# Kernel tuning notes

Measured on AMD Instinct MI355X. Metric: run time of the kernel, lower is better.

## Reference

```python
import jax, jax.numpy as jnp
import numpy as np

L, C, H = 4, 512, 8
HD = C // H

def silu(x):
    return x * jax.nn.sigmoid(x)

def layernorm(x, g, b, eps=1e-5):
    m = x.mean(-1, keepdims=True)
    v = ((x - m) ** 2).mean(-1, keepdims=True)
    return (x - m) * jax.lax.rsqrt(v + eps) * g + b

def adaln(x, t, w, b):
    # x: (N,B,C), t: (B,C), w: (2C,C), b: (2C,)
    mod = silu(t) @ w.T + b
    scale, shift = jnp.split(mod, 2, axis=-1)
    return x * (1.0 + scale[None]) + shift[None]

def embed_rotary(x, pos):
    # x: (B,N,C), pos: (B,N,C,2) with [...,0]=cos, [...,1]=sin
    cos, sin = pos[..., 0], pos[..., 1]
    x2 = jnp.stack([-x[..., 1::2], x[..., 0::2]], axis=-1).reshape(x.shape)
    return x * cos + x2 * sin

def setup_inputs() -> dict:
    key = jax.random.key(0)
    ks = jax.random.split(key, 24)
    Nq, Nkv, B = 1024, 2048, 4
    query = jax.random.normal(ks[0], (Nq, B, C), jnp.float32)
    value = jax.random.normal(ks[1], (Nkv, B, C), jnp.float32)
    diff_ts = jax.random.normal(ks[2], (B, C), jnp.float32)
    # valid rotary codes: cos/sin of random angles
    aq = jax.random.uniform(ks[3], (B, Nq, C), jnp.float32, 0.0, 2 * np.pi)
    ak = jax.random.uniform(ks[4], (B, Nkv, C), jnp.float32, 0.0, 2 * np.pi)
    query_pos = jnp.stack([jnp.cos(aq), jnp.sin(aq)], axis=-1)
    value_pos = jnp.stack([jnp.cos(ak), jnp.sin(ak)], axis=-1)
    s = 0.02
    inp = dict(query=query, value=value, diff_ts=diff_ts,
               query_pos=query_pos, value_pos=value_pos,
               aw_attn=jax.random.normal(ks[5], (L, 2 * C, C)) * s,
               ab_attn=jax.random.normal(ks[6], (L, 2 * C)) * s,
               in_w=jax.random.normal(ks[7], (L, 3 * C, C)) * s,
               in_b=jnp.zeros((L, 3 * C)),
               out_w=jax.random.normal(ks[8], (L, C, C)) * s,
               out_b=jnp.zeros((L, C)),
               ln1_g=jnp.ones((L, C)), ln1_b=jnp.zeros((L, C)),
               aw_ffn=jax.random.normal(ks[9], (L, 2 * C, C)) * s,
               ab_ffn=jax.random.normal(ks[10], (L, 2 * C)) * s,
               w1=jax.random.normal(ks[11], (L, C, C)) * s,
               b1=jnp.zeros((L, C)),
               w2=jax.random.normal(ks[12], (L, C, C)) * s,
               b2=jnp.zeros((L, C)),
               ln2_g=jnp.ones((L, C)), ln2_b=jnp.zeros((L, C)))
    return inp

def _forward(query, value, diff_ts, query_pos, value_pos,
             aw_attn, ab_attn, in_w, in_b, out_w, out_b, ln1_g, ln1_b,
             aw_ffn, ab_ffn, w1, b1, w2, b2, ln2_g, ln2_b):
    Nq, B, _ = query.shape
    Nkv = value.shape[0]
    scaling = HD ** -0.5
    outputs = []
    q = query
    for i in range(L):
        # --- cross-attention layer ---
        aq = adaln(q, diff_ts, aw_attn[i], ab_attn[i])
        wq, wk, wv = jnp.split(in_w[i], 3, axis=0)
        bq, bk, bv = jnp.split(in_b[i], 3, axis=0)
        qp = (aq @ wq.T + bq) * scaling          # (Nq,B,C)
        kp = value @ wk.T + bk                    # (Nkv,B,C)
        vp = value @ wv.T + bv
        qb = embed_rotary(qp.transpose(1, 0, 2), query_pos)  # (B,Nq,C)
        kb = embed_rotary(kp.transpose(1, 0, 2), value_pos)  # (B,Nkv,C)
        vb = vp.transpose(1, 0, 2)
        qh = qb.reshape(B, Nq, H, HD).transpose(0, 2, 1, 3)   # (B,H,Nq,HD)
        kh = kb.reshape(B, Nkv, H, HD).transpose(0, 2, 1, 3)
        vh = vb.reshape(B, Nkv, H, HD).transpose(0, 2, 1, 3)
        scores = jnp.einsum('bhqd,bhkd->bhqk', qh, kh)
        attn = jax.nn.softmax(scores, axis=-1)
        o = jnp.einsum('bhqk,bhkd->bhqd', attn, vh)
        o = o.transpose(0, 2, 1, 3).reshape(B, Nq, C).transpose(1, 0, 2)  # (Nq,B,C)
        o = o @ out_w[i].T + out_b[i]
        q = layernorm(q + o, ln1_g[i], ln1_b[i])
        # --- feedforward layer (residual uses AdaLN-modulated x) ---
        xa = adaln(q, diff_ts, aw_ffn[i], ab_ffn[i])
        h = jax.nn.relu(xa @ w1[i].T + b1[i])
        h = h @ w2[i].T + b2[i]
        q = layernorm(xa + h, ln2_g[i], ln2_b[i])
        outputs.append(q)
    return jnp.stack(outputs)  # (L, Nq, B, C)

def reference(query, value, diff_ts, query_pos, value_pos,
              aw_attn, ab_attn, in_w, in_b, out_w, out_b, ln1_g, ln1_b,
              aw_ffn, ab_ffn, w1, b1, w2, b2, ln2_g, ln2_b):
    return _forward(query, value, diff_ts, query_pos, value_pos,
                    aw_attn, ab_attn, in_w, in_b, out_w, out_b, ln1_g, ln1_b,
                    aw_ffn, ab_ffn, w1, b1, w2, b2, ln2_g, ln2_b)
```

## Files before the change

kernel.cpp:

```cpp
#include <hip/hip_runtime.h>
#include <hip/hip_bf16.h>

typedef __hip_bfloat16 bf16;
typedef __attribute__((ext_vector_type(8))) short short8;
typedef __attribute__((ext_vector_type(4))) float f32x4;

#define CDIM 512
#define BDIM 4
#define HDIM 8
#define HDQ  64
#define NQ   1024
#define NKV  2048
#define LAYERS 4
#define SPLIT 2

#if defined(__has_builtin)
#if __has_builtin(__builtin_amdgcn_global_load_lds)
#define USE_GLL 1
#endif
#endif

static __device__ __forceinline__ short f2s(float f) {
    bf16 h = __float2bfloat16(f);
    return *reinterpret_cast<short*>(&h);
}


__global__ __launch_bounds__(256) void conv_f2b(const float* __restrict__ in,
                                                bf16* __restrict__ out, int n) {
    int i = blockIdx.x * 256 + threadIdx.x;
    if (i < n) out[i] = __float2bfloat16(in[i]);
}

__global__ __launch_bounds__(256) void silu_k(const float* __restrict__ t,
                                              float* __restrict__ st) {
    int i = blockIdx.x * 256 + threadIdx.x;
    float x = t[i];
    st[i] = x / (1.f + __expf(-x));
}

__global__ __launch_bounds__(256) void modall_k(const float* __restrict__ st,
    const float* __restrict__ aw_attn, const float* __restrict__ ab_attn,
    const float* __restrict__ aw_ffn,  const float* __restrict__ ab_ffn,
    float* __restrict__ mod) {
    int idx = blockIdx.x * 256 + threadIdx.x;
    int col  = idx & 1023;
    int b    = (idx >> 10) & 3;
    int kind = (idx >> 12) & 1;
    int l    = idx >> 13;
    const float* w = (kind ? aw_ffn : aw_attn) + ((size_t)l * 1024 + col) * CDIM;
    float acc = (kind ? ab_ffn : ab_attn)[l * 1024 + col];
    const float* tb = st + b * CDIM;
    for (int k = 0; k < CDIM; ++k) acc += tb[k] * w[k];
    mod[idx] = acc;
}

__global__ __launch_bounds__(256) void adaln_k(const float* __restrict__ x,
                                               const float* __restrict__ mod,
                                               bf16* __restrict__ outb) {
    int i = blockIdx.x * 256 + threadIdx.x;
    int c = i & 511;
    int b = (i >> 9) & 3;
    outb[i] = __float2bfloat16(x[i] * (1.f + mod[b * 1024 + c]) + mod[b * 1024 + 512 + c]);
}

__global__ __launch_bounds__(256) void ln_ad_k(const float* __restrict__ x,
                                               const float* __restrict__ res,
                                               const float* __restrict__ g,
                                               const float* __restrict__ bb,
                                               const float* __restrict__ mod,
                                               float* __restrict__ ln_f,
                                               float* __restrict__ ln_f2,
                                               float* __restrict__ ad_f,
                                               bf16* __restrict__ ad_b) {
    int row = blockIdx.x;
    int t = threadIdx.x;
    size_t base = (size_t)row * CDIM;
    float v0 = x[base + t] + res[base + t];
    float v1 = x[base + t + 256] + res[base + t + 256];
    float s1 = v0 + v1;
    float s2 = v0 * v0 + v1 * v1;
    #pragma unroll
    for (int off = 32; off; off >>= 1) {
        s1 += __shfl_xor(s1, off);
        s2 += __shfl_xor(s2, off);
    }
    __shared__ float a1[4], a2[4];
    int w = t >> 6;
    if ((t & 63) == 0) { a1[w] = s1; a2[w] = s2; }
    __syncthreads();
    s1 = a1[0] + a1[1] + a1[2] + a1[3];
    s2 = a2[0] + a2[1] + a2[2] + a2[3];
    float mean = s1 * (1.f / 512.f);
    float var = s2 * (1.f / 512.f) - mean * mean;
    float rs = rsqrtf(var + 1e-5f);
    float y0 = (v0 - mean) * rs * g[t] + bb[t];
    float y1 = (v1 - mean) * rs * g[t + 256] + bb[t + 256];
    if (ln_f)  { ln_f[base + t] = y0;  ln_f[base + t + 256] = y1; }
    if (ln_f2) { ln_f2[base + t] = y0; ln_f2[base + t + 256] = y1; }
    if (mod) {
        int b = row & 3;
        float o0 = y0 * (1.f + mod[b * 1024 + t]) + mod[b * 1024 + 512 + t];
        float o1 = y1 * (1.f + mod[b * 1024 + t + 256]) + mod[b * 1024 + 512 + t + 256];
        if (ad_f) { ad_f[base + t] = o0; ad_f[base + t + 256] = o1; }
        ad_b[base + t] = __float2bfloat16(o0);
        ad_b[base + t + 256] = __float2bfloat16(o1);
    }
}

template <int EPI, int WM, int NT>
__global__ __launch_bounds__(256) void mgemm_k(
    const bf16* __restrict__ A, const bf16* __restrict__ Wt,
    const float* __restrict__ bias, void* __restrict__ out0v,
    void* __restrict__ out1v, int M, int N, int K,
    const float* __restrict__ pos, float scl, int Nseq) {
    __shared__ bf16 As[WM * 32 * 32];
    __shared__ bf16 Bs[NT * 32 * 32];
    const int BM = WM * 32;
    const int BN = NT * 32;
    int t = threadIdx.x;
    int w = t >> 6;
    int lane = t & 63;
    int l16 = lane & 15;
    int quad = lane >> 4;
    int wy = w >> 1, wx = w & 1;
    int bm = blockIdx.y * BM;
    int bn = blockIdx.x * BN;
#if USE_GLL
    int lr = lane >> 2;
    int lq = lane & 3;
#endif

    f32x4 acc[WM][NT] = {};

    for (int k0 = 0; k0 < K; k0 += 32) {
        __syncthreads();
#if USE_GLL
        if (w < 2) {
            const bf16* src = A + (size_t)(bm + w * (WM * 16)) * K + k0;
            bf16* dstb = As + (w * (WM * 16)) * 32;
            #pragma unroll
            for (int i = 0; i < WM; ++i) {
                __builtin_amdgcn_global_load_lds(
                    (const unsigned int __attribute__((address_space(1)))*)
                        (src + ((size_t)(i * 16 + lr)) * K + lq * 8),
                    (unsigned int __attribute__((address_space(3)))*)
                        (dstb + i * 16 * 32),
                    16, 0, 0);
            }
        } else {
            const bf16* src = Wt + (size_t)(bn + (w - 2) * (NT * 16)) * K + k0;
            bf16* dstb = Bs + ((w - 2) * (NT * 16)) * 32;
            #pragma unroll
            for (int i = 0; i < NT; ++i) {
                __builtin_amdgcn_global_load_lds(
                    (const unsigned int __attribute__((address_space(1)))*)
                        (src + ((size_t)(i * 16 + lr)) * K + lq * 8),
                    (unsigned int __attribute__((address_space(3)))*)
                        (dstb + i * 16 * 32),
                    16, 0, 0);
            }
        }
#else
        for (int e = t; e < BM * 4; e += 256) {
            int row = e >> 2, kq = e & 3;
            *(uint4*)&As[row * 32 + kq * 8] =
                *(const uint4*)(A + (size_t)(bm + row) * K + k0 + kq * 8);
        }
        for (int e = t; e < BN * 4; e += 256) {
            int row = e >> 2, kq = e & 3;
            *(uint4*)&Bs[row * 32 + kq * 8] =
                *(const uint4*)(Wt + (size_t)(bn + row) * K + k0 + kq * 8);
        }
#endif
        __syncthreads();

        short8 af[WM], bfr[NT];
        #pragma unroll
        for (int mt = 0; mt < WM; ++mt)
            af[mt] = *(const short8*)&As[((wy * WM + mt) * 16 + l16) * 32 + quad * 8];
        #pragma unroll
        for (int nt = 0; nt < NT; ++nt)
            bfr[nt] = *(const short8*)&Bs[((wx * NT + nt) * 16 + l16) * 32 + quad * 8];
        #pragma unroll
        for (int mt = 0; mt < WM; ++mt)
            #pragma unroll
            for (int nt = 0; nt < NT; ++nt)
                acc[mt][nt] = __builtin_amdgcn_mfma_f32_16x16x32_bf16(
                    af[mt], bfr[nt], acc[mt][nt], 0, 0, 0);
    }

    #pragma unroll
    for (int nt = 0; nt < NT; ++nt) {
        int n = bn + (wx * NT + nt) * 16 + l16;
        float bnv = (EPI == 4) ? 0.f : bias[n];
        #pragma unroll
        for (int mt = 0; mt < WM; ++mt) {
            #pragma unroll
            for (int r = 0; r < 4; ++r) {
                int m = bm + (wy * WM + mt) * 16 + quad * 4 + r;
                float v = acc[mt][nt][r] + ((EPI == 4) ? bias[m] : bnv);
                if (EPI == 0) {
                    ((float*)out0v)[(size_t)m * N + n] = v;
                } else if (EPI == 1) {
                    ((bf16*)out0v)[(size_t)m * N + n] = __float2bfloat16(fmaxf(v, 0.f));
                } else if (EPI == 4) {
                    int hh = m >> 6, dd = m & 63;
                    int bsel = n & 3, key = n >> 2;
                    ((bf16*)out0v)[((size_t)(bsel * HDIM + hh) * HDQ + dd) * NKV + key] =
                        __float2bfloat16(v);
                } else {
                    v *= scl;
                    int c = n;
                    int nseq = m >> 2, b = m & 3;
                    float part = __shfl_xor(v, 1);
                    const float* pp = pos + (((size_t)b * Nseq + nseq) * CDIM + c) * 2;
                    float cs = pp[0], sn = pp[1];
                    float o = (l16 & 1) ? (v * cs + part * sn) : (v * cs - part * sn);
                    bf16* op = (bf16*)out0v +
                               ((size_t)(b * HDIM + (c >> 6)) * Nseq + nseq) * HDQ + (c & 63);
                    *op = __float2bfloat16(o);
                }
            }
        }
    }
}

__global__ __launch_bounds__(256) void attn4_k(const bf16* __restrict__ qh,
                                               const bf16* __restrict__ kh,
                                               const bf16* __restrict__ vT,
                                               float* __restrict__ pl,
                                               float* __restrict__ pacc) {
    __shared__ short Ks[64][72];
    __shared__ short VsT[64][72];
    __shared__ short Ps[4][16][72];
    int t = threadIdx.x;
    int wave = t >> 6, lane = t & 63;
    int l16 = lane & 15, quad = lane >> 4;
    int bh = blockIdx.y;
    int q0 = blockIdx.x * 64 + wave * 16;
    int kbase = blockIdx.z * (NKV / SPLIT);

    const bf16* qbase = qh + ((size_t)bh * NQ + q0) * HDQ;
    short8 aq0 = *(const short8*)(qbase + (size_t)l16 * HDQ + quad * 8);
    short8 aq1 = *(const short8*)(qbase + (size_t)l16 * HDQ + 32 + quad * 8);
    const bf16* kbh = kh + ((size_t)bh * NKV + kbase) * HDQ;
    const bf16* vbh = vT + (size_t)bh * HDQ * NKV + kbase;

    f32x4 accO[4] = {};
    float lsum[4] = {0.f, 0.f, 0.f, 0.f};

    for (int kt = 0; kt < NKV / SPLIT; kt += 64) {
        __syncthreads();
        #pragma unroll
        for (int i = 0; i < 2; ++i) {
            int idx = t + i * 256;
            int row = idx >> 3, c8 = (idx & 7) * 8;
            *(short8*)&Ks[row][c8] =
                *(const short8*)(kbh + (size_t)(kt + row) * HDQ + c8);
            *(short8*)&VsT[row][c8] =
                *(const short8*)(vbh + (size_t)row * NKV + kt + c8);
        }
        __syncthreads();

        f32x4 sc[4] = {};
        #pragma unroll
        for (int nt = 0; nt < 4; ++nt) {
            short8 bk0 = *(const short8*)&Ks[nt * 16 + l16][quad * 8];
            short8 bk1 = *(const short8*)&Ks[nt * 16 + l16][32 + quad * 8];
            sc[nt] = __builtin_amdgcn_mfma_f32_16x16x32_bf16(aq0, bk0, sc[nt], 0, 0, 0);
            sc[nt] = __builtin_amdgcn_mfma_f32_16x16x32_bf16(aq1, bk1, sc[nt], 0, 0, 0);
        }

        #pragma unroll
        for (int r = 0; r < 4; ++r) {
            float p0 = exp2f(sc[0][r] * 1.44269504f);
            float p1 = exp2f(sc[1][r] * 1.44269504f);
            float p2 = exp2f(sc[2][r] * 1.44269504f);
            float p3 = exp2f(sc[3][r] * 1.44269504f);
            lsum[r] += (p0 + p1) + (p2 + p3);
            int pr = quad * 4 + r;
            Ps[wave][pr][l16]      = f2s(p0);
            Ps[wave][pr][16 + l16] = f2s(p1);
            Ps[wave][pr][32 + l16] = f2s(p2);
            Ps[wave][pr][48 + l16] = f2s(p3);
        }

        short8 pa0 = *(const short8*)&Ps[wave][l16][quad * 8];
        short8 pa1 = *(const short8*)&Ps[wave][l16][32 + quad * 8];
        #pragma unroll
        for (int nt = 0; nt < 4; ++nt) {
            short8 bv0 = *(const short8*)&VsT[nt * 16 + l16][quad * 8];
            short8 bv1 = *(const short8*)&VsT[nt * 16 + l16][32 + quad * 8];
            accO[nt] = __builtin_amdgcn_mfma_f32_16x16x32_bf16(pa0, bv0, accO[nt], 0, 0, 0);
            accO[nt] = __builtin_amdgcn_mfma_f32_16x16x32_bf16(pa1, bv1, accO[nt], 0, 0, 0);
        }
    }

    #pragma unroll
    for (int r = 0; r < 4; ++r) {
        #pragma unroll
        for (int off = 1; off < 16; off <<= 1) lsum[r] += __shfl_xor(lsum[r], off);
    }

    size_t rowbase = ((size_t)blockIdx.z * 32 + bh) * NQ + q0;
    #pragma unroll
    for (int r = 0; r < 4; ++r) {
        size_t row = rowbase + quad * 4 + r;
        if (l16 == 0) pl[row] = lsum[r];
        #pragma unroll
        for (int nt = 0; nt < 4; ++nt)
            pacc[row * 64 + nt * 16 + l16] = accO[nt][r];
    }
}

__global__ __launch_bounds__(256) void attn_comb_k(const float* __restrict__ pl,
                                                   const float* __restrict__ pacc,
                                                   bf16* __restrict__ o) {
    int idx = blockIdx.x * 256 + threadIdx.x;
    int d = idx & 63;
    int row = idx >> 6;
    int q = row & (NQ - 1);
    int bh = row >> 10;
    const int S = 32 * NQ;
    float l = pl[row] + pl[S + row];
    float v = pacc[(size_t)row * 64 + d] + pacc[(size_t)(S + row) * 64 + d];
    int b = bh >> 3, h = bh & 7;
    o[((size_t)(q * BDIM + b)) * CDIM + h * HDQ + d] = __float2bfloat16(v / l);
}


extern "C" void kernel_launch(void* const* d_in, const int* in_sizes, int n_in,
                              void* d_out, int out_size, void* d_ws, size_t ws_size,
                              hipStream_t stream) {
    const float* query     = (const float*)d_in[0];
    const float* value     = (const float*)d_in[1];
    const float* diff_ts   = (const float*)d_in[2];
    const float* query_pos = (const float*)d_in[3];
    const float* value_pos = (const float*)d_in[4];
    const float* aw_attn   = (const float*)d_in[5];
    const float* ab_attn   = (const float*)d_in[6];
    const float* in_w      = (const float*)d_in[7];
    const float* in_b      = (const float*)d_in[8];
    const float* out_w     = (const float*)d_in[9];
    const float* out_b     = (const float*)d_in[10];
    const float* ln1_g     = (const float*)d_in[11];
    const float* ln1_b     = (const float*)d_in[12];
    const float* aw_ffn    = (const float*)d_in[13];
    const float* ab_ffn    = (const float*)d_in[14];
    const float* w1        = (const float*)d_in[15];
    const float* b1        = (const float*)d_in[16];
    const float* w2        = (const float*)d_in[17];
    const float* b2        = (const float*)d_in[18];
    const float* ln2_g     = (const float*)d_in[19];
    const float* ln2_b     = (const float*)d_in[20];
    float* out_f = (float*)d_out;

    float* ws      = (float*)d_ws;
    float* st      = ws;
    float* mod_ws  = ws + 2048;
    float* q_cur   = ws + 34816;
    float* buf_a   = q_cur + 2097152;
    float* buf_p   = buf_a + 2097152;
    bf16* a_bf     = (bf16*)(buf_p + 2097152);
    bf16* h_bf     = a_bf + 2097152;
    bf16* qh       = h_bf + 2097152;
    bf16* kh       = qh + 2097152;
    bf16* vt       = kh + 4194304;
    bf16* val_bf   = vt + 4194304;
    bf16* winb     = val_bf + 4194304;
    bf16* woutb    = winb + 3145728;
    bf16* w1b      = woutb + 1048576;
    bf16* w2b      = w1b + 1048576;
    float* pacc    = buf_a;
    float* pl      = (float*)a_bf;

    const int MQ = NQ * BDIM;
    const int MKV = NKV * BDIM;
    const float scaling = 0.125f;

    silu_k<<<8, 256, 0, stream>>>(diff_ts, st);
    modall_k<<<128, 256, 0, stream>>>(st, aw_attn, ab_attn, aw_ffn, ab_ffn, mod_ws);
    conv_f2b<<<16384, 256, 0, stream>>>(value, val_bf, 4194304);
    conv_f2b<<<12288, 256, 0, stream>>>(in_w, winb, 3145728);
    conv_f2b<<<4096, 256, 0, stream>>>(out_w, woutb, 1048576);
    conv_f2b<<<4096, 256, 0, stream>>>(w1, w1b, 1048576);
    conv_f2b<<<4096, 256, 0, stream>>>(w2, w2b, 1048576);
    adaln_k<<<(MQ * CDIM) / 256, 256, 0, stream>>>(query, mod_ws, a_bf);

    for (int i = 0; i < LAYERS; ++i) {
        const float* mod_ffn  = mod_ws + i * 8192 + 4096;
        const float* mod_attn_next = (i + 1 < LAYERS) ? (mod_ws + (i + 1) * 8192) : nullptr;
        const bf16* winb_i = winb + (size_t)i * 1536 * CDIM;
        const float* in_b_i = in_b + (size_t)i * 1536;
        const float* qsrc = (i == 0) ? query : q_cur;

        mgemm_k<2, 2, 2><<<dim3(8, MQ / 64), 256, 0, stream>>>(
            a_bf, winb_i, in_b_i, qh, nullptr, MQ, 512, CDIM, query_pos, scaling, NQ);
        mgemm_k<2, 2, 2><<<dim3(8, MKV / 64), 256, 0, stream>>>(
            val_bf, winb_i + (size_t)512 * CDIM, in_b_i + 512, kh, nullptr, MKV, 512,
            CDIM, value_pos, 1.f, NKV);
        mgemm_k<4, 2, 2><<<dim3(MKV / 64, 8), 256, 0, stream>>>(
            winb_i + (size_t)1024 * CDIM, val_bf, in_b_i + 1024, vt, nullptr,
            512, MKV, CDIM, nullptr, 0.f, 0);
        attn4_k<<<dim3(NQ / 64, BDIM * HDIM, SPLIT), 256, 0, stream>>>(
            qh, kh, vt, pl, pacc);
        attn_comb_k<<<8192, 256, 0, stream>>>(pl, pacc, h_bf);
        mgemm_k<0, 2, 2><<<dim3(8, MQ / 64), 256, 0, stream>>>(
            h_bf, woutb + (size_t)i * CDIM * CDIM, out_b + i * CDIM, buf_p, nullptr,
            MQ, 512, CDIM, nullptr, 0.f, 0);
        ln_ad_k<<<MQ, 256, 0, stream>>>(qsrc, buf_p, ln1_g + i * CDIM, ln1_b + i * CDIM,
                                        mod_ffn, nullptr, nullptr, buf_a, a_bf);
        mgemm_k<1, 2, 2><<<dim3(8, MQ / 64), 256, 0, stream>>>(
            a_bf, w1b + (size_t)i * CDIM * CDIM, b1 + i * CDIM, h_bf, nullptr,
            MQ, 512, CDIM, nullptr, 0.f, 0);
        mgemm_k<0, 2, 2><<<dim3(8, MQ / 64), 256, 0, stream>>>(
            h_bf, w2b + (size_t)i * CDIM * CDIM, b2 + i * CDIM, buf_p, nullptr,
            MQ, 512, CDIM, nullptr, 0.f, 0);
        ln_ad_k<<<MQ, 256, 0, stream>>>(buf_a, buf_p, ln2_g + i * CDIM, ln2_b + i * CDIM,
                                        mod_attn_next, q_cur,
                                        out_f + (size_t)i * MQ * CDIM, nullptr, a_bf);
    }
}
```

Before: 783.8 us.

## Double-buffer GEMM and attention tiles, swizzle LDS, parallelize modulation matvec

Turns the modulation matvec from one thread per output looping over 512 inputs into one wave per output with vectorized loads and a shuffle reduction. The GEMM and attention kernels gain double-buffered LDS staging, so the next tile is fetched while MFMAs run on the current one, with one barrier per iteration. Attention replaces padded LDS rows with an XOR swizzle to avoid bank conflicts, and the log2(e) factor is folded into the query scaling so the exp multiply disappears. Double buffering raises LDS use per block, which may lower occupancy.

```diff
diff --git a/kernel.cpp b/kernel.cpp
--- a/kernel.cpp
+++ b/kernel.cpp
@@ -43,16 +43,24 @@
     const float* __restrict__ aw_attn, const float* __restrict__ ab_attn,
     const float* __restrict__ aw_ffn,  const float* __restrict__ ab_ffn,
     float* __restrict__ mod) {
-    int idx = blockIdx.x * 256 + threadIdx.x;
-    int col  = idx & 1023;
-    int b    = (idx >> 10) & 3;
-    int kind = (idx >> 12) & 1;
-    int l    = idx >> 13;
-    const float* w = (kind ? aw_ffn : aw_attn) + ((size_t)l * 1024 + col) * CDIM;
-    float acc = (kind ? ab_ffn : ab_attn)[l * 1024 + col];
-    const float* tb = st + b * CDIM;
-    for (int k = 0; k < CDIM; ++k) acc += tb[k] * w[k];
-    mod[idx] = acc;
+    int wv = blockIdx.x * 4 + (threadIdx.x >> 6);
+    int lane = threadIdx.x & 63;
+    int col  = wv & 1023;
+    int b    = (wv >> 10) & 3;
+    int kind = (wv >> 12) & 1;
+    int l    = wv >> 13;
+    const float* w = (kind ? aw_ffn : aw_attn) + ((size_t)l * 1024 + col) * CDIM + lane * 8;
+    const float* tb = st + b * CDIM + lane * 8;
+    f32x4 w0 = *(const f32x4*)w;
+    f32x4 w1 = *(const f32x4*)(w + 4);
+    f32x4 t0 = *(const f32x4*)tb;
+    f32x4 t1 = *(const f32x4*)(tb + 4);
+    f32x4 pp = w0 * t0 + w1 * t1;
+    float acc = (pp[0] + pp[1]) + (pp[2] + pp[3]);
+    #pragma unroll
+    for (int off = 32; off; off >>= 1) acc += __shfl_xor(acc, off);
+    if (lane == 0)
+        mod[wv] = acc + (kind ? ab_ffn : ab_attn)[l * 1024 + col];
 }
 
 __global__ __launch_bounds__(256) void adaln_k(const float* __restrict__ x,
@@ -114,8 +122,8 @@
     const float* __restrict__ bias, void* __restrict__ out0v,
     void* __restrict__ out1v, int M, int N, int K,
     const float* __restrict__ pos, float scl, int Nseq) {
-    __shared__ bf16 As[WM * 32 * 32];
-    __shared__ bf16 Bs[NT * 32 * 32];
+    __shared__ bf16 As[2][WM * 32 * 32];
+    __shared__ bf16 Bs[2][NT * 32 * 32];
     const int BM = WM * 32;
     const int BN = NT * 32;
     int t = threadIdx.x;
@@ -133,12 +141,11 @@
 
     f32x4 acc[WM][NT] = {};
 
-    for (int k0 = 0; k0 < K; k0 += 32) {
-        __syncthreads();
+    auto stage = [&](int buf, int k0) {
 #if USE_GLL
         if (w < 2) {
             const bf16* src = A + (size_t)(bm + w * (WM * 16)) * K + k0;
-            bf16* dstb = As + (w * (WM * 16)) * 32;
+            bf16* dstb = As[buf] + (w * (WM * 16)) * 32;
             #pragma unroll
             for (int i = 0; i < WM; ++i) {
                 __builtin_amdgcn_global_load_lds(
@@ -150,7 +157,7 @@
             }
         } else {
             const bf16* src = Wt + (size_t)(bn + (w - 2) * (NT * 16)) * K + k0;
-            bf16* dstb = Bs + ((w - 2) * (NT * 16)) * 32;
+            bf16* dstb = Bs[buf] + ((w - 2) * (NT * 16)) * 32;
             #pragma unroll
             for (int i = 0; i < NT; ++i) {
                 __builtin_amdgcn_global_load_lds(
@@ -164,30 +171,40 @@
 #else
         for (int e = t; e < BM * 4; e += 256) {
             int row = e >> 2, kq = e & 3;
-            *(uint4*)&As[row * 32 + kq * 8] =
+            *(uint4*)&As[buf][row * 32 + kq * 8] =
                 *(const uint4*)(A + (size_t)(bm + row) * K + k0 + kq * 8);
         }
         for (int e = t; e < BN * 4; e += 256) {
             int row = e >> 2, kq = e & 3;
-            *(uint4*)&Bs[row * 32 + kq * 8] =
+            *(uint4*)&Bs[buf][row * 32 + kq * 8] =
                 *(const uint4*)(Wt + (size_t)(bn + row) * K + k0 + kq * 8);
         }
 #endif
-        __syncthreads();
+    };
+
+    stage(0, 0);
+    __syncthreads();
+    int cur = 0;
+
+    for (int k0 = 0; k0 < K; k0 += 32) {
+        if (k0 + 32 < K) stage(cur ^ 1, k0 + 32);
 
         short8 af[WM], bfr[NT];
         #pragma unroll
         for (int mt = 0; mt < WM; ++mt)
-            af[mt] = *(const short8*)&As[((wy * WM + mt) * 16 + l16) * 32 + quad * 8];
+            af[mt] = *(const short8*)&As[cur][((wy * WM + mt) * 16 + l16) * 32 + quad * 8];
         #pragma unroll
         for (int nt = 0; nt < NT; ++nt)
-            bfr[nt] = *(const short8*)&Bs[((wx * NT + nt) * 16 + l16) * 32 + quad * 8];
+            bfr[nt] = *(const short8*)&Bs[cur][((wx * NT + nt) * 16 + l16) * 32 + quad * 8];
         #pragma unroll
         for (int mt = 0; mt < WM; ++mt)
             #pragma unroll
             for (int nt = 0; nt < NT; ++nt)
                 acc[mt][nt] = __builtin_amdgcn_mfma_f32_16x16x32_bf16(
                     af[mt], bfr[nt], acc[mt][nt], 0, 0, 0);
+
+        __syncthreads();
+        cur ^= 1;
     }
 
     #pragma unroll
@@ -231,9 +248,9 @@
                                                const bf16* __restrict__ vT,
                                                float* __restrict__ pl,
                                                float* __restrict__ pacc) {
-    __shared__ short Ks[64][72];
-    __shared__ short VsT[64][72];
-    __shared__ short Ps[4][16][72];
+    __shared__ short Kb[2][64 * 64];
+    __shared__ short Vb[2][64 * 64];
+    __shared__ short Ps[4][16 * 64];
     int t = threadIdx.x;
     int wave = t >> 6, lane = t & 63;
     int l16 = lane & 15, quad = lane >> 4;
@@ -247,54 +264,91 @@
     const bf16* kbh = kh + ((size_t)bh * NKV + kbase) * HDQ;
     const bf16* vbh = vT + (size_t)bh * HDQ * NKV + kbase;
 
+    int r0 = wave * 16;
+    int lr = lane >> 3;
+    int swz_src = ((lane & 7) ^ lr) * 8;
+
+    auto stage = [&](int buf, int kt) {
+#if USE_GLL
+        #pragma unroll
+        for (int j = 0; j < 2; ++j) {
+            int rr = r0 + j * 8;
+            __builtin_amdgcn_global_load_lds(
+                (const unsigned int __attribute__((address_space(1)))*)
+                    (kbh + (size_t)(kt + rr + lr) * HDQ + swz_src),
+                (unsigned int __attribute__((address_space(3)))*)&Kb[buf][rr * 64],
+                16, 0, 0);
+            __builtin_amdgcn_global_load_lds(
+                (const unsigned int __attribute__((address_space(1)))*)
+                    (vbh + (size_t)(rr + lr) * NKV + kt + swz_src),
+                (unsigned int __attribute__((address_space(3)))*)&Vb[buf][rr * 64],
+                16, 0, 0);
+        }
+#else
+        #pragma unroll
+        for (int j = 0; j < 2; ++j) {
+            int rr = r0 + j * 8 + lr;
+            int lc = lane & 7;
+            *(short8*)&Kb[buf][rr * 64 + ((lc ^ (rr & 7)) * 8)] =
+                *(const short8*)(kbh + (size_t)(kt + rr) * HDQ + lc * 8);
+            *(short8*)&Vb[buf][rr * 64 + ((lc ^ (rr & 7)) * 8)] =
+                *(const short8*)(vbh + (size_t)rr * NKV + kt + lc * 8);
+        }
+#endif
+    };
+
     f32x4 accO[4] = {};
     float lsum[4] = {0.f, 0.f, 0.f, 0.f};
 
+    stage(0, 0);
+    __syncthreads();
+    int cur = 0;
+    int swz_m = l16 & 7;
+
     for (int kt = 0; kt < NKV / SPLIT; kt += 64) {
-        __syncthreads();
-        #pragma unroll
-        for (int i = 0; i < 2; ++i) {
-            int idx = t + i * 256;
-            int row = idx >> 3, c8 = (idx & 7) * 8;
-            *(short8*)&Ks[row][c8] =
-                *(const short8*)(kbh + (size_t)(kt + row) * HDQ + c8);
-            *(short8*)&VsT[row][c8] =
-                *(const short8*)(vbh + (size_t)row * NKV + kt + c8);
-        }
-        __syncthreads();
+        if (kt + 64 < NKV / SPLIT) stage(cur ^ 1, kt + 64);
 
         f32x4 sc[4] = {};
         #pragma unroll
         for (int nt = 0; nt < 4; ++nt) {
-            short8 bk0 = *(const short8*)&Ks[nt * 16 + l16][quad * 8];
-            short8 bk1 = *(const short8*)&Ks[nt * 16 + l16][32 + quad * 8];
+            const short* kr = &Kb[cur][(nt * 16 + l16) * 64];
+            short8 bk0 = *(const short8*)&kr[(quad ^ swz_m) * 8];
+            short8 bk1 = *(const short8*)&kr[((quad + 4) ^ swz_m) * 8];
             sc[nt] = __builtin_amdgcn_mfma_f32_16x16x32_bf16(aq0, bk0, sc[nt], 0, 0, 0);
             sc[nt] = __builtin_amdgcn_mfma_f32_16x16x32_bf16(aq1, bk1, sc[nt], 0, 0, 0);
         }
 
         #pragma unroll
         for (int r = 0; r < 4; ++r) {
-            float p0 = exp2f(sc[0][r] * 1.44269504f);
-            float p1 = exp2f(sc[1][r] * 1.44269504f);
-            float p2 = exp2f(sc[2][r] * 1.44269504f);
-            float p3 = exp2f(sc[3][r] * 1.44269504f);
+            float p0 = exp2f(sc[0][r]);
+            float p1 = exp2f(sc[1][r]);
+            float p2 = exp2f(sc[2][r]);
+            float p3 = exp2f(sc[3][r]);
             lsum[r] += (p0 + p1) + (p2 + p3);
             int pr = quad * 4 + r;
-            Ps[wave][pr][l16]      = f2s(p0);
-            Ps[wave][pr][16 + l16] = f2s(p1);
-            Ps[wave][pr][32 + l16] = f2s(p2);
-            Ps[wave][pr][48 + l16] = f2s(p3);
-        }
-
-        short8 pa0 = *(const short8*)&Ps[wave][l16][quad * 8];
-        short8 pa1 = *(const short8*)&Ps[wave][l16][32 + quad * 8];
+            short* prow = &Ps[wave][pr * 64];
+            int pm = pr & 7;
+            int ch = l16 >> 3, kl = l16 & 7;
+            prow[((ch ^ pm) << 3) + kl]       = f2s(p0);
+            prow[(((ch + 2) ^ pm) << 3) + kl] = f2s(p1);
+            prow[(((ch + 4) ^ pm) << 3) + kl] = f2s(p2);
+            prow[(((ch + 6) ^ pm) << 3) + kl] = f2s(p3);
+        }
+
+        const short* prd = &Ps[wave][l16 * 64];
+        short8 pa0 = *(const short8*)&prd[(quad ^ swz_m) * 8];
+        short8 pa1 = *(const short8*)&prd[((quad + 4) ^ swz_m) * 8];
         #pragma unroll
         for (int nt = 0; nt < 4; ++nt) {
-            short8 bv0 = *(const short8*)&VsT[nt * 16 + l16][quad * 8];
-            short8 bv1 = *(const short8*)&VsT[nt * 16 + l16][32 + quad * 8];
+            const short* vr = &Vb[cur][(nt * 16 + l16) * 64];
+            short8 bv0 = *(const short8*)&vr[(quad ^ swz_m) * 8];
+            short8 bv1 = *(const short8*)&vr[((quad + 4) ^ swz_m) * 8];
             accO[nt] = __builtin_amdgcn_mfma_f32_16x16x32_bf16(pa0, bv0, accO[nt], 0, 0, 0);
             accO[nt] = __builtin_amdgcn_mfma_f32_16x16x32_bf16(pa1, bv1, accO[nt], 0, 0, 0);
         }
+
+        __syncthreads();
+        cur ^= 1;
     }
 
     #pragma unroll
@@ -377,10 +431,10 @@
 
     const int MQ = NQ * BDIM;
     const int MKV = NKV * BDIM;
-    const float scaling = 0.125f;
+    const float scaling = 0.125f * 1.44269504f;
 
     silu_k<<<8, 256, 0, stream>>>(diff_ts, st);
-    modall_k<<<128, 256, 0, stream>>>(st, aw_attn, ab_attn, aw_ffn, ab_ffn, mod_ws);
+    modall_k<<<8192, 256, 0, stream>>>(st, aw_attn, ab_attn, aw_ffn, ab_ffn, mod_ws);
     conv_f2b<<<16384, 256, 0, stream>>>(value, val_bf, 4194304);
     conv_f2b<<<12288, 256, 0, stream>>>(in_w, winb, 3145728);
     conv_f2b<<<4096, 256, 0, stream>>>(out_w, woutb, 1048576);
```

New measurement: 729.7 us. 1.07x faster.
